# Optimization experiments

Measured on AMD Instinct MI355X. Metric: run time of the kernel, lower is better.

The kernel has to match this reference:

```python
import jax, jax.numpy as jnp
import numpy as np

N_NODES = 50000
N_EDGES = 800000
N_GRAPHS = 256
D_IN = 128
D_HID = 128


def setup_inputs() -> dict:
    key = jax.random.key(0)
    ks = jax.random.split(key, 10)
    x = jax.random.normal(ks[0], (N_NODES, D_IN), dtype=jnp.float32)
    edge_index = jax.random.randint(ks[1], (2, N_EDGES), 0, N_NODES, dtype=jnp.int64)
    batch = jnp.sort(jax.random.randint(ks[2], (N_NODES,), 0, N_GRAPHS, dtype=jnp.int64))
    def lin(k, din, dout):
        s = 1.0 / np.sqrt(din)
        return jax.random.uniform(k, (din, dout), jnp.float32, -s, s)
    W1 = lin(ks[3], D_IN, D_HID); b1 = jnp.zeros((D_HID,), jnp.float32)
    W2 = lin(ks[4], D_HID, D_HID); b2 = jnp.zeros((D_HID,), jnp.float32)
    W3 = lin(ks[5], D_HID, D_HID); b3 = jnp.zeros((D_HID,), jnp.float32)
    return {"x": x, "edge_index": edge_index, "batch": batch,
            "W1": W1, "b1": b1, "W2": W2, "b2": b2, "W3": W3, "b3": b3}


def _gcn_norm(edge_index, num_nodes):
    # PyG gcn_norm with add_self_loops=True, edge_weight=1
    loops = jnp.arange(num_nodes, dtype=edge_index.dtype)
    src = jnp.concatenate([edge_index[0], loops])
    dst = jnp.concatenate([edge_index[1], loops])
    ones = jnp.ones(src.shape[0], jnp.float32)
    deg = jax.ops.segment_sum(ones, dst, num_segments=num_nodes)
    dinv = jnp.where(deg > 0, jax.lax.rsqrt(deg), 0.0)
    norm = dinv[src] * dinv[dst]
    return src, dst, norm


def _gcn_conv(x, src, dst, norm, W, b, num_nodes):
    h = x @ W                              # [N, dout] transform first
    msg = h[src] * norm[:, None]           # gather + scale  [E+N, dout]
    agg = jax.ops.segment_sum(msg, dst, num_segments=num_nodes)
    return agg + b


def reference(x, edge_index, batch, W1, b1, W2, b2, W3, b3):
    n = x.shape[0]
    src, dst, norm = _gcn_norm(edge_index, n)
    h = jax.nn.relu(_gcn_conv(x, src, dst, norm, W1, b1, n))
    h = jax.nn.relu(_gcn_conv(h, src, dst, norm, W2, b2, n))
    h = _gcn_conv(h, src, dst, norm, W3, b3, n)
    # global_mean_pool over batch ids
    sums = jax.ops.segment_sum(h, batch, num_segments=N_GRAPHS)
    cnts = jax.ops.segment_sum(jnp.ones((n,), jnp.float32), batch, num_segments=N_GRAPHS)
    return sums / jnp.maximum(cnts, 1.0)[:, None]
```

## Files before the change

kernel.cpp:

```cpp
#include <hip/hip_runtime.h>

#define N_NODES 50000
#define N_PAD   50048
#define N_EDGES 800000
#define N_GRAPHS 256
#define D 128
#define CAP 64
#define GEMM_GRID (N_PAD / 64)

#define NBUCK 196
#define BCAP  4608
#define EPB_I4 512
#define NBLK_A ((N_EDGES / 4 + EPB_I4 - 1) / EPB_I4)

typedef short bf16x8 __attribute__((ext_vector_type(8)));
typedef float f32x4  __attribute__((ext_vector_type(4)));

__device__ inline unsigned short f2bf(float f) {
    unsigned u = __float_as_uint(f);
    u += 0x7FFF + ((u >> 16) & 1);
    return (unsigned short)(u >> 16);
}
__device__ inline float bf2f(unsigned short b) { return __uint_as_float((unsigned)b << 16); }

__global__ __launch_bounds__(256) void k_pack(const float* __restrict__ W1, const float* __restrict__ W2,
                                              const float* __restrict__ W3, unsigned short* __restrict__ Wp) {
    int idx = blockIdx.x * 256 + threadIdx.x;
    if (idx >= 3 * D * D) return;
    int L = idx >> 14, rem = idx & 16383;
    int k = rem >> 7, n = rem & 127;
    const float* W = (L == 0) ? W1 : (L == 1) ? W2 : W3;
    float w = W[k * D + n];
    int kt = k >> 5, kg = (k >> 3) & 3, i = k & 7;
    int nt = n >> 4, ln = kg * 16 + (n & 15);
    size_t dst = (size_t)L * 32768 + ((size_t)(kt * 8 + nt) * 64 + ln) * 8 + i;
    unsigned short hi = f2bf(w);
    Wp[dst]         = hi;
    Wp[dst + 16384] = f2bf(w - bf2f(hi));
}


__global__ __launch_bounds__(256) void k_part(const int* __restrict__ ei, int* __restrict__ cursor,
                                              unsigned* __restrict__ buck) {
    __shared__ int hist[NBUCK];
    __shared__ int lbase[NBUCK];
    for (int i = threadIdx.x; i < NBUCK; i += 256) hist[i] = 0;
    __syncthreads();

    const int4* s4 = reinterpret_cast<const int4*>(ei);
    const int4* d4 = reinterpret_cast<const int4*>(ei + N_EDGES);
    int idx0 = blockIdx.x * EPB_I4 + threadIdx.x;
    int idx1 = idx0 + 256;
    bool v0 = idx0 < N_EDGES / 4, v1 = idx1 < N_EDGES / 4;
    int4 d0 = {}, d1 = {}, s0 = {}, s1 = {};
    if (v0) {
        d0 = d4[idx0]; s0 = s4[idx0];
        atomicAdd(&hist[d0.x >> 8], 1); atomicAdd(&hist[d0.y >> 8], 1);
        atomicAdd(&hist[d0.z >> 8], 1); atomicAdd(&hist[d0.w >> 8], 1);
    }
    if (v1) {
        d1 = d4[idx1]; s1 = s4[idx1];
        atomicAdd(&hist[d1.x >> 8], 1); atomicAdd(&hist[d1.y >> 8], 1);
        atomicAdd(&hist[d1.z >> 8], 1); atomicAdd(&hist[d1.w >> 8], 1);
    }
    __syncthreads();

    for (int i = threadIdx.x; i < NBUCK; i += 256)
        lbase[i] = atomicAdd(&cursor[i], hist[i]);
    __syncthreads();

    auto put = [&](int d, int s) {
        int b = d >> 8;
        int p = atomicAdd(&lbase[b], 1);
        if (p < BCAP) buck[(size_t)b * BCAP + p] = ((unsigned)(d & 255) << 16) | (unsigned)s;
    };
    if (v0) { put(d0.x, s0.x); put(d0.y, s0.y); put(d0.z, s0.z); put(d0.w, s0.w); }
    if (v1) { put(d1.x, s1.x); put(d1.y, s1.y); put(d1.z, s1.z); put(d1.w, s1.w); }
}


__global__ __launch_bounds__(256) void k_build(const unsigned* __restrict__ buck,
                                               const int* __restrict__ cursor,
                                               int* __restrict__ cnt, unsigned short* __restrict__ colu) {
    __shared__ int lcnt[256];
    int b = blockIdx.x;
    lcnt[threadIdx.x] = 0;
    __syncthreads();
    int nE = min(cursor[b], BCAP);
    const unsigned* bb = buck + (size_t)b * BCAP;
    for (int i = threadIdx.x; i < nE; i += 256) {
        unsigned v = bb[i];
        int dl = v >> 16, s = v & 0xFFFF;
        int p = atomicAdd(&lcnt[dl], 1);
        if (p < CAP) colu[(size_t)(b * 256 + dl) * CAP + p] = (unsigned short)s;
    }
    __syncthreads();
    int node = b * 256 + threadIdx.x;
    if (node < N_NODES) cnt[node] = lcnt[threadIdx.x];
}


template<bool F32IN>
__global__ __launch_bounds__(256) void k_mfma(const void* __restrict__ Ain,
                                              const unsigned short* __restrict__ Wp,
                                              const int* __restrict__ cnt,
                                              unsigned short* __restrict__ T) {
    int l  = threadIdx.x & 63;
    int wv = threadIdx.x >> 6;
    int row0 = blockIdx.x * 64 + wv * 16;
    int arow = row0 + (l & 15);
    int kchunk = l >> 4;
    const uint4* wp4 = reinterpret_cast<const uint4*>(Wp);

    f32x4 acc[8] = {};
    #pragma unroll
    for (int s = 0; s < 4; ++s) {
        bf16x8 af;
        if (F32IN) {
            float4 a0 = {}, a1 = {};
            if (arow < N_NODES) {
                const float* xr = (const float*)Ain + (size_t)arow * D + s * 32 + kchunk * 8;
                a0 = reinterpret_cast<const float4*>(xr)[0];
                a1 = reinterpret_cast<const float4*>(xr)[1];
            }
            unsigned short h[8] = { f2bf(a0.x), f2bf(a0.y), f2bf(a0.z), f2bf(a0.w),
                                    f2bf(a1.x), f2bf(a1.y), f2bf(a1.z), f2bf(a1.w) };
            __builtin_memcpy(&af, h, 16);
        } else {
            const unsigned short* ar = (const unsigned short*)Ain + (size_t)arow * D;
            uint4 av = reinterpret_cast<const uint4*>(ar)[s * 4 + kchunk];
            __builtin_memcpy(&af, &av, 16);
        }
        #pragma unroll
        for (int nt = 0; nt < 8; ++nt) {
            int f = s * 8 + nt;
            uint4 bh = wp4[f * 64 + l];
            uint4 bl = wp4[f * 64 + l + 2048];
            bf16x8 bhf, blf;
            __builtin_memcpy(&bhf, &bh, 16);
            __builtin_memcpy(&blf, &bl, 16);
            acc[nt] = __builtin_amdgcn_mfma_f32_16x16x32_bf16(af, bhf, acc[nt], 0, 0, 0);
            acc[nt] = __builtin_amdgcn_mfma_f32_16x16x32_bf16(af, blf, acc[nt], 0, 0, 0);
        }
    }

    int rbase = row0 + (l >> 4) * 4;
    int cr = l & 15;
    float sc[4];
    #pragma unroll
    for (int j = 0; j < 4; ++j) {
        int rr = rbase + j;
        sc[j] = (rr < N_NODES) ? rsqrtf((float)cnt[rr] + 1.f) : 0.f;
    }
    #pragma unroll
    for (int nt = 0; nt < 8; ++nt)
        #pragma unroll
        for (int j = 0; j < 4; ++j) {
            int rr = rbase + j;
            if (rr < N_NODES) T[(size_t)rr * D + nt * 16 + cr] = f2bf(acc[nt][j] * sc[j]);
        }
}


template<bool LAST>
__global__ __launch_bounds__(256) void k_agg(const unsigned* __restrict__ Tu, float* __restrict__ AGG,
                                             unsigned* __restrict__ Anext, const float* __restrict__ bias,
                                             const int* __restrict__ cnt, const unsigned short* __restrict__ colu) {
    int node = blockIdx.x * 4 + (threadIdx.x >> 6);
    int lane = threadIdx.x & 63;
    if (node >= N_NODES) return;

    int len = cnt[node];
    float dd = rsqrtf((float)len + 1.f);
    unsigned ts = Tu[(size_t)node * 64 + lane];
    float2 acc;
    acc.x = __uint_as_float(ts << 16);
    acc.y = __uint_as_float(ts & 0xFFFF0000u);

    const unsigned short* crow = colu + (size_t)node * CAP;
    int j = 0;
    for (; j + 8 <= len; j += 8) {
        uint4 c = *reinterpret_cast<const uint4*>(crow + j);
        int s0 = c.x & 0xFFFF, s1 = c.x >> 16;
        int s2 = c.y & 0xFFFF, s3 = c.y >> 16;
        int s4 = c.z & 0xFFFF, s5 = c.z >> 16;
        int s6 = c.w & 0xFFFF, s7 = c.w >> 16;
        unsigned t0 = Tu[(size_t)s0 * 64 + lane];
        unsigned t1 = Tu[(size_t)s1 * 64 + lane];
        unsigned t2 = Tu[(size_t)s2 * 64 + lane];
        unsigned t3 = Tu[(size_t)s3 * 64 + lane];
        unsigned t4 = Tu[(size_t)s4 * 64 + lane];
        unsigned t5 = Tu[(size_t)s5 * 64 + lane];
        unsigned t6 = Tu[(size_t)s6 * 64 + lane];
        unsigned t7 = Tu[(size_t)s7 * 64 + lane];
        acc.x += __uint_as_float(t0 << 16); acc.y += __uint_as_float(t0 & 0xFFFF0000u);
        acc.x += __uint_as_float(t1 << 16); acc.y += __uint_as_float(t1 & 0xFFFF0000u);
        acc.x += __uint_as_float(t2 << 16); acc.y += __uint_as_float(t2 & 0xFFFF0000u);
        acc.x += __uint_as_float(t3 << 16); acc.y += __uint_as_float(t3 & 0xFFFF0000u);
        acc.x += __uint_as_float(t4 << 16); acc.y += __uint_as_float(t4 & 0xFFFF0000u);
        acc.x += __uint_as_float(t5 << 16); acc.y += __uint_as_float(t5 & 0xFFFF0000u);
        acc.x += __uint_as_float(t6 << 16); acc.y += __uint_as_float(t6 & 0xFFFF0000u);
        acc.x += __uint_as_float(t7 << 16); acc.y += __uint_as_float(t7 & 0xFFFF0000u);
    }
    for (; j < len; ++j) {
        int s = crow[j];
        unsigned t0 = Tu[(size_t)s * 64 + lane];
        acc.x += __uint_as_float(t0 << 16); acc.y += __uint_as_float(t0 & 0xFFFF0000u);
    }

    acc.x *= dd; acc.y *= dd;
    if (!LAST) {
        float rx = fmaxf(acc.x + bias[2 * lane], 0.f);
        float ry = fmaxf(acc.y + bias[2 * lane + 1], 0.f);
        Anext[(size_t)node * 64 + lane] = (unsigned)f2bf(rx) | ((unsigned)f2bf(ry) << 16);
    } else {
        reinterpret_cast<float2*>(AGG)[(size_t)node * 64 + lane] = acc;
    }
}


__global__ __launch_bounds__(128) void k_pool(const float* __restrict__ AGG, const float* __restrict__ b3,
                                              const int* __restrict__ batch, float* __restrict__ out) {
    int g = blockIdx.x;
    int c = threadIdx.x;
    int beg, end;
    { int lo = 0, hi = N_NODES; while (lo < hi) { int m = (lo + hi) >> 1; if (batch[m] < g) lo = m + 1; else hi = m; } beg = lo; }
    { int lo = beg, hi = N_NODES; while (lo < hi) { int m = (lo + hi) >> 1; if (batch[m] < g + 1) lo = m + 1; else hi = m; } end = lo; }
    float acc = 0.f;
    #pragma unroll 4
    for (int i = beg; i < end; ++i) acc += AGG[(size_t)i * D + c];
    int n = end - beg;
    out[g * D + c] = (acc + (float)n * b3[c]) / (float)(n > 0 ? n : 1);
}


static inline size_t align256(size_t x) { return (x + 255) & ~(size_t)255; }

extern "C" void kernel_launch(void* const* d_in, const int* in_sizes, int n_in,
                              void* d_out, int out_size, void* d_ws, size_t ws_size,
                              hipStream_t stream) {
    const float* x    = (const float*)d_in[0];
    const int*  ei    = (const int*)d_in[1];
    const int*  batch = (const int*)d_in[2];
    const float* W1 = (const float*)d_in[3];
    const float* b1 = (const float*)d_in[4];
    const float* W2 = (const float*)d_in[5];
    const float* b2 = (const float*)d_in[6];
    const float* W3 = (const float*)d_in[7];
    const float* b3 = (const float*)d_in[8];
    float* out = (float*)d_out;

    char* ws = (char*)d_ws;
    size_t off = 0;
    auto alloc = [&](size_t bytes) { void* p = ws + off; off = align256(off + bytes); return p; };
    int*      cursor = (int*)     alloc((size_t)NBUCK * 4);
    unsigned* buck   = (unsigned*)alloc((size_t)NBUCK * BCAP * 4);
    int*      cnt    = (int*)     alloc((size_t)N_NODES * 4);
    unsigned short* colu = (unsigned short*)alloc((size_t)NBUCK * 256 * CAP * 2);
    unsigned short* Wp = (unsigned short*)alloc((size_t)3 * 32768 * 2);
    unsigned short* Ab = (unsigned short*)alloc((size_t)N_PAD * D * 2);
    unsigned short* T  = (unsigned short*)alloc((size_t)N_PAD * D * 2);
    float* AGG  = (float*)alloc((size_t)N_NODES * D * 4);
    (void)ws_size; (void)in_sizes; (void)n_in; (void)out_size;

    hipMemsetAsync(cursor, 0, (size_t)NBUCK * 4, stream);

    k_pack <<<(3 * D * D + 255) / 256, 256, 0, stream>>>(W1, W2, W3, Wp);
    k_part <<<NBLK_A, 256, 0, stream>>>(ei, cursor, buck);
    k_build<<<NBUCK, 256, 0, stream>>>(buck, cursor, cnt, colu);

    const int agg_grid = (N_NODES + 3) / 4;

    k_mfma<true ><<<GEMM_GRID, 256, 0, stream>>>(x,  Wp,         cnt, T);
    k_agg<false><<<agg_grid, 256, 0, stream>>>((const unsigned*)T, nullptr, (unsigned*)Ab, b1, cnt, colu);
    k_mfma<false><<<GEMM_GRID, 256, 0, stream>>>(Ab, Wp + 32768, cnt, T);
    k_agg<false><<<agg_grid, 256, 0, stream>>>((const unsigned*)T, nullptr, (unsigned*)Ab, b2, cnt, colu);
    k_mfma<false><<<GEMM_GRID, 256, 0, stream>>>(Ab, Wp + 65536, cnt, T);
    k_agg<true ><<<agg_grid, 256, 0, stream>>>((const unsigned*)T, AGG, nullptr, nullptr, cnt, colu);
    k_pool <<<N_GRAPHS, 128, 0, stream>>>(AGG, b3, batch, out);
}
```

Baseline: 293.8 us.

## Stage weights in LDS for MFMA and store final aggregation as bf16

The MFMA GEMM kernel now uses 512-thread blocks covering 128 rows. Each block copies the 64 KB packed weight slice into shared memory once and reads B fragments from LDS rather than global memory. The final aggregation layer writes bf16 into the reused Ab buffer instead of an fp32 AGG buffer, and the pooling kernel reads bf16. This halves the final-layer write and the pool's read traffic, at the cost of precision in the pooled sums and lower occupancy from 64 KB of LDS per block.

```diff
diff --git a/kernel.cpp b/kernel.cpp
--- a/kernel.cpp
+++ b/kernel.cpp
@@ -6,7 +6,7 @@
 #define N_GRAPHS 256
 #define D 128
 #define CAP 64
-#define GEMM_GRID (N_PAD / 64)
+#define MFMA_GRID (N_PAD / 128)
 
 #define NBUCK 196
 #define BCAP  4608
@@ -101,16 +101,20 @@
 
 
 template<bool F32IN>
-__global__ __launch_bounds__(256) void k_mfma(const void* __restrict__ Ain,
+__global__ __launch_bounds__(512) void k_mfma(const void* __restrict__ Ain,
                                               const unsigned short* __restrict__ Wp,
                                               const int* __restrict__ cnt,
                                               unsigned short* __restrict__ T) {
+    __shared__ uint4 Wl[4096];
+    const uint4* wp4 = reinterpret_cast<const uint4*>(Wp);
+    for (int i = threadIdx.x; i < 4096; i += 512) Wl[i] = wp4[i];
+    __syncthreads();
+
     int l  = threadIdx.x & 63;
     int wv = threadIdx.x >> 6;
-    int row0 = blockIdx.x * 64 + wv * 16;
+    int row0 = blockIdx.x * 128 + wv * 16;
     int arow = row0 + (l & 15);
     int kchunk = l >> 4;
-    const uint4* wp4 = reinterpret_cast<const uint4*>(Wp);
 
     f32x4 acc[8] = {};
     #pragma unroll
@@ -134,8 +138,8 @@
         #pragma unroll
         for (int nt = 0; nt < 8; ++nt) {
             int f = s * 8 + nt;
-            uint4 bh = wp4[f * 64 + l];
-            uint4 bl = wp4[f * 64 + l + 2048];
+            uint4 bh = Wl[f * 64 + l];
+            uint4 bl = Wl[f * 64 + l + 2048];
             bf16x8 bhf, blf;
             __builtin_memcpy(&bhf, &bh, 16);
             __builtin_memcpy(&blf, &bl, 16);
@@ -163,7 +167,7 @@
 
 
 template<bool LAST>
-__global__ __launch_bounds__(256) void k_agg(const unsigned* __restrict__ Tu, float* __restrict__ AGG,
+__global__ __launch_bounds__(256) void k_agg(const unsigned* __restrict__ Tu,
                                              unsigned* __restrict__ Anext, const float* __restrict__ bias,
                                              const int* __restrict__ cnt, const unsigned short* __restrict__ colu) {
     int node = blockIdx.x * 4 + (threadIdx.x >> 6);
@@ -210,16 +214,15 @@
 
     acc.x *= dd; acc.y *= dd;
     if (!LAST) {
-        float rx = fmaxf(acc.x + bias[2 * lane], 0.f);
-        float ry = fmaxf(acc.y + bias[2 * lane + 1], 0.f);
-        Anext[(size_t)node * 64 + lane] = (unsigned)f2bf(rx) | ((unsigned)f2bf(ry) << 16);
-    } else {
-        reinterpret_cast<float2*>(AGG)[(size_t)node * 64 + lane] = acc;
-    }
-}
-
-
-__global__ __launch_bounds__(128) void k_pool(const float* __restrict__ AGG, const float* __restrict__ b3,
+        acc.x = fmaxf(acc.x + bias[2 * lane], 0.f);
+        acc.y = fmaxf(acc.y + bias[2 * lane + 1], 0.f);
+    }
+    Anext[(size_t)node * 64 + lane] = (unsigned)f2bf(acc.x) | ((unsigned)f2bf(acc.y) << 16);
+}
+
+
+__global__ __launch_bounds__(128) void k_pool(const unsigned short* __restrict__ AGGb,
+                                              const float* __restrict__ b3,
                                               const int* __restrict__ batch, float* __restrict__ out) {
     int g = blockIdx.x;
     int c = threadIdx.x;
@@ -228,7 +231,7 @@
     { int lo = beg, hi = N_NODES; while (lo < hi) { int m = (lo + hi) >> 1; if (batch[m] < g + 1) lo = m + 1; else hi = m; } end = lo; }
     float acc = 0.f;
     #pragma unroll 4
-    for (int i = beg; i < end; ++i) acc += AGG[(size_t)i * D + c];
+    for (int i = beg; i < end; ++i) acc += bf2f(AGGb[(size_t)i * D + c]);
     int n = end - beg;
     out[g * D + c] = (acc + (float)n * b3[c]) / (float)(n > 0 ? n : 1);
 }
@@ -260,7 +263,6 @@
     unsigned short* Wp = (unsigned short*)alloc((size_t)3 * 32768 * 2);
     unsigned short* Ab = (unsigned short*)alloc((size_t)N_PAD * D * 2);
     unsigned short* T  = (unsigned short*)alloc((size_t)N_PAD * D * 2);
-    float* AGG  = (float*)alloc((size_t)N_NODES * D * 4);
     (void)ws_size; (void)in_sizes; (void)n_in; (void)out_size;
 
     hipMemsetAsync(cursor, 0, (size_t)NBUCK * 4, stream);
@@ -271,11 +273,11 @@
 
     const int agg_grid = (N_NODES + 3) / 4;
 
-    k_mfma<true ><<<GEMM_GRID, 256, 0, stream>>>(x,  Wp,         cnt, T);
-    k_agg<false><<<agg_grid, 256, 0, stream>>>((const unsigned*)T, nullptr, (unsigned*)Ab, b1, cnt, colu);
-    k_mfma<false><<<GEMM_GRID, 256, 0, stream>>>(Ab, Wp + 32768, cnt, T);
-    k_agg<false><<<agg_grid, 256, 0, stream>>>((const unsigned*)T, nullptr, (unsigned*)Ab, b2, cnt, colu);
-    k_mfma<false><<<GEMM_GRID, 256, 0, stream>>>(Ab, Wp + 65536, cnt, T);
-    k_agg<true ><<<agg_grid, 256, 0, stream>>>((const unsigned*)T, AGG, nullptr, nullptr, cnt, colu);
-    k_pool <<<N_GRAPHS, 128, 0, stream>>>(AGG, b3, batch, out);
-}
+    k_mfma<true ><<<MFMA_GRID, 512, 0, stream>>>(x,  Wp,         cnt, T);
+    k_agg<false><<<agg_grid, 256, 0, stream>>>((const unsigned*)T, (unsigned*)Ab, b1, cnt, colu);
+    k_mfma<false><<<MFMA_GRID, 512, 0, stream>>>(Ab, Wp + 32768, cnt, T);
+    k_agg<false><<<agg_grid, 256, 0, stream>>>((const unsigned*)T, (unsigned*)Ab, b2, cnt, colu);
+    k_mfma<false><<<MFMA_GRID, 512, 0, stream>>>(Ab, Wp + 65536, cnt, T);
+    k_agg<true ><<<agg_grid, 256, 0, stream>>>((const unsigned*)T, (unsigned*)Ab, nullptr, cnt, colu);
+    k_pool <<<N_GRAPHS, 128, 0, stream>>>(Ab, b3, batch, out);
+}
```

New measurement: 276.3 us. -5.9%, faster.
